# Optimization experiments

Measured on AMD Instinct MI355X. Metric: run time of the kernel, lower is better.

Reference implementation:

```python
import jax, jax.numpy as jnp
import numpy as np

# Dimensions
T, B = 128, 512
NTOK, NINP, NHID = 512, 512, 600
NB, BS, TOPK = 6, 100, 4          # num_blocks, block_size = nhid//num_blocks, update_topk
H, DK, DV, ATT = 4, 64, 85, 340   # input-attention heads, key dim, value dim (H*DV == attention_out)
H2, DK2, DV2 = 4, 32, 32          # communication (step) attention dims


def setup_inputs() -> dict:
    key = jax.random.key(0)
    ks = jax.random.split(key, 16)
    def rn(k, shape, s=0.05):
        return (jax.random.normal(k, shape) * s).astype(jnp.float32)
    return dict(
        input=jax.random.normal(ks[0], (T, B, NTOK), dtype=jnp.float32),
        h0=jnp.zeros((B, NHID), jnp.float32),
        masks=jnp.ones((T, B, 1), jnp.float32),
        enc_W=rn(ks[1], (NTOK, NINP)), enc_b=jnp.zeros((NINP,), jnp.float32),
        Wq_in=rn(ks[2], (BS, H * DK)), Wk_in=rn(ks[3], (NINP, H * DK)), Wv_in=rn(ks[4], (NINP, H * DV)),
        W_ih=rn(ks[5], (NB, ATT, 3 * BS)), W_hh=rn(ks[6], (NB, BS, 3 * BS)),
        b_ih=jnp.zeros((NB, 3 * BS), jnp.float32), b_hh=jnp.zeros((NB, 3 * BS), jnp.float32),
        Wq_c=rn(ks[7], (BS, H2 * DK2)), Wk_c=rn(ks[8], (BS, H2 * DK2)),
        Wv_c=rn(ks[9], (BS, H2 * DV2)), Wo_c=rn(ks[10], (H2 * DV2, BS)),
        dec_W=rn(ks[11], (NHID, NTOK)), dec_b=jnp.zeros((NTOK,), jnp.float32),
    )


def _rim_scan(emb, masks, h0, Wq_in, Wk_in, Wv_in, W_ih, W_hh, b_ih, b_hh,
              Wq_c, Wk_c, Wv_c, Wo_c):
    inv_sdk = 1.0 / np.sqrt(DK).astype(np.float32)
    inv_sdk2 = 1.0 / np.sqrt(DK2).astype(np.float32)

    def step(h, xm):
        xt, mt = xm                      # [B,NINP], [B,1]
        h = h * mt                       # episode-reset gating
        hb = h.reshape(B, NB, BS)
        # --- input attention over {real input, null} slots ---
        slots = jnp.stack([xt, jnp.zeros_like(xt)], axis=1)          # [B,2,NINP]
        k = (slots @ Wk_in).reshape(B, 2, H, DK)
        v = (slots @ Wv_in).reshape(B, 2, H, DV)
        q = (hb @ Wq_in).reshape(B, NB, H, DK)
        att = jax.nn.softmax(jnp.einsum('bnhd,bshd->bnhs', q, k) * inv_sdk, axis=-1)
        act = 1.0 - att[..., 1].mean(-1)                             # [B,NB] attention to real input
        kth = jax.lax.top_k(act, TOPK)[0][:, -1:]
        mask = (act >= kth).astype(h.dtype)                          # [B,NB] top-k block activation
        inp_use = jnp.einsum('bnhs,bshd->bnhd', att, v).reshape(B, NB, ATT)
        # --- block-diagonal GRU update ---
        gi = jnp.einsum('bnd,nde->bne', inp_use, W_ih) + b_ih
        gh = jnp.einsum('bnd,nde->bne', hb, W_hh) + b_hh
        gi_r, gi_z, gi_n = jnp.split(gi, 3, axis=-1)
        gh_r, gh_z, gh_n = jnp.split(gh, 3, axis=-1)
        r = jax.nn.sigmoid(gi_r + gh_r)
        z = jax.nn.sigmoid(gi_z + gh_z)
        n = jnp.tanh(gi_n + r * gh_n)
        hn = (1.0 - z) * n + z * hb
        # --- step (communication) attention across blocks, residual ---
        qc = (hn @ Wq_c).reshape(B, NB, H2, DK2)
        kc = (hn @ Wk_c).reshape(B, NB, H2, DK2)
        vc = (hn @ Wv_c).reshape(B, NB, H2, DV2)
        ac = jax.nn.softmax(jnp.einsum('bnhd,bmhd->bhnm', qc, kc) * inv_sdk2, axis=-1)
        co = jnp.einsum('bhnm,bmhd->bnhd', ac, vc).reshape(B, NB, H2 * DV2) @ Wo_c
        hc = hn + co
        # --- only top-k active blocks are updated ---
        m = mask[..., None]
        hf = (m * hc + (1.0 - m) * hb).reshape(B, NHID)
        return hf, (hf, mask)

    h_last, (hs, bmask) = jax.lax.scan(step, h0, (emb, masks))
    return hs, h_last, bmask


def reference(input, h0, masks, enc_W, enc_b, Wq_in, Wk_in, Wv_in,
              W_ih, W_hh, b_ih, b_hh, Wq_c, Wk_c, Wv_c, Wo_c, dec_W, dec_b):
    emb = input @ enc_W + enc_b                                      # encoder Linear [T,B,NINP]
    hs, h_last, bmask = _rim_scan(emb, masks, h0, Wq_in, Wk_in, Wv_in,
                                  W_ih, W_hh, b_ih, b_hh, Wq_c, Wk_c, Wv_c, Wo_c)
    dec = hs @ dec_W + dec_b                                         # decoder [T,B,NTOK]
    return dec
```

## Files before the change

kernel.cpp:

```cpp
#include <hip/hip_runtime.h>
#include <math.h>

#define T_STEPS 128
#define BATCH   512
#define NTOK    512
#define NINP    512
#define NHID    600
#define NBK     6
#define BS      100
#define HH      4
#define DK      64
#define DV      85
#define ATT     340
#define H2      4
#define DK2     32
#define DV2     32
#define G3      300
#define VN      340
#define KAPN    400
#define CN      740
#define CNP     768
#define UN2     1800
#define UN2P    1920
#define UK0     128
#define KV0     512
#define DECKP   640
#define SW      2

typedef __attribute__((ext_vector_type(8))) short short8;
typedef __attribute__((ext_vector_type(4))) float f32x4;

__device__ __forceinline__ float sigf(float x) { return 1.f / (1.f + expf(-x)); }
__device__ __forceinline__ unsigned short f2b(float f) {
    unsigned u = __float_as_uint(f);
    unsigned r = (u + 0x7fffu + ((u >> 16) & 1u)) >> 16;
    return (unsigned short)r;
}
__device__ __forceinline__ float b2f(unsigned short u) {
    return __uint_as_float(((unsigned)u) << 16);
}
__device__ __forceinline__ void split3(float x, unsigned short& hi,
                                       unsigned short& mid, unsigned short& lo) {
    hi = f2b(x);
    float r1 = x - b2f(hi);
    mid = f2b(r1);
    lo = f2b(r1 - b2f(mid));
}

struct ZOff { int div; long s1; long s2; };
__device__ __forceinline__ long zoff(ZOff z, int bz) {
    return (long)(bz / z.div) * z.s1 + (long)(bz % z.div) * z.s2;
}

__device__ __forceinline__ void swz_decode(int& x, int& y, int& z) {
    int gx = gridDim.x, gy = gridDim.y;
    int flat = (blockIdx.z * gy + blockIdx.y) * gx + blockIdx.x;
    int nwg = gx * gy * gridDim.z;
    int per = nwg >> 3;
    int nf = (flat & 7) * per + (flat >> 3);
    y = nf % gy; int t2 = nf / gy; x = t2 % gx; z = t2 / gx;
}

__global__ __launch_bounds__(256) void gemm6(
    const unsigned short* __restrict__ A, long aZ, int aZdiv,
    const unsigned short* __restrict__ B, long bZ,
    float* __restrict__ C, long cZ, int ldc, int Nreal,
    const float* __restrict__ bias, int K0)
{
    int bx, by, bz;
    swz_decode(bx, by, bz);
    A += (long)(bz / aZdiv) * aZ;
    B += (long)bz * bZ;
    C += (long)bz * cZ;
    const int LDA = 3 * K0;
    const int m0 = by * 128, n0 = bx * 128;
    __shared__ __align__(16) unsigned short As[128 * 64];
    __shared__ __align__(16) unsigned short Bs[128 * 64];
    const int tid = threadIdx.x;
    const int lane = tid & 63;
    const int wid = tid >> 6;
    const int wr = wid >> 1, wc = wid & 1;

    f32x4 acc[4][4];
#pragma unroll
    for (int m = 0; m < 4; m++)
#pragma unroll
        for (int n = 0; n < 4; n++)
#pragma unroll
            for (int v = 0; v < 4; v++) acc[m][n][v] = 0.f;

    const int segA[6] = {0, 0, 1, 0, 2, 1};
    const int segB[6] = {0, 1, 0, 2, 0, 1};
    for (int p = 0; p < 6; p++) {
        const unsigned short* Ap = A + segA[p] * K0;
        const unsigned short* Bp = B + segB[p] * K0;
        for (int k0 = 0; k0 < K0; k0 += 64) {
            short8 ra[4], rb[4];
#pragma unroll
            for (int q = 0; q < 4; q++) {
                int idx = (q << 8) + tid;
                int r = idx >> 3, ce = (idx & 7) << 3;
                ra[q] = *(const short8*)&Ap[(long)(m0 + r) * LDA + k0 + ce];
                rb[q] = *(const short8*)&Bp[(long)(n0 + r) * LDA + k0 + ce];
            }
            __syncthreads();
#pragma unroll
            for (int q = 0; q < 4; q++) {
                int idx = (q << 8) + tid;
                int r = idx >> 3, ce = (idx & 7) << 3;
                *(short8*)&As[r * 64 + ce] = ra[q];
                *(short8*)&Bs[r * 64 + ce] = rb[q];
            }
            __syncthreads();
#pragma unroll
            for (int kk = 0; kk < 2; kk++) {
                short8 af[4], bfr[4];
#pragma unroll
                for (int m = 0; m < 4; m++)
                    af[m] = *(const short8*)&As[(wr * 64 + m * 16 + (lane & 15)) * 64 + kk * 32 + (lane >> 4) * 8];
#pragma unroll
                for (int n = 0; n < 4; n++)
                    bfr[n] = *(const short8*)&Bs[(wc * 64 + n * 16 + (lane & 15)) * 64 + kk * 32 + (lane >> 4) * 8];
#pragma unroll
                for (int m = 0; m < 4; m++)
#pragma unroll
                    for (int n = 0; n < 4; n++)
                        acc[m][n] = __builtin_amdgcn_mfma_f32_16x16x32_bf16(af[m], bfr[n], acc[m][n], 0, 0, 0);
            }
        }
    }
#pragma unroll
    for (int m = 0; m < 4; m++) {
        int rbase = m0 + wr * 64 + m * 16 + (lane >> 4) * 4;
#pragma unroll
        for (int n = 0; n < 4; n++) {
            int col = n0 + wc * 64 + n * 16 + (lane & 15);
            if (col < Nreal) {
                float bv = bias ? bias[col] : 0.f;
#pragma unroll
                for (int v = 0; v < 4; v++)
                    C[(long)(rbase + v) * ldc + col] = acc[m][n][v] + bv;
            }
        }
    }
}

__global__ __launch_bounds__(256) void gemm6_kv(
    const unsigned short* __restrict__ A,
    const unsigned short* __restrict__ B,
    unsigned short* __restrict__ A_U,
    float* __restrict__ Kbuf,
    const float* __restrict__ bias, int K0, int MU)
{
    int bx, by, bz;
    swz_decode(bx, by, bz);
    const int LDA = 3 * K0;
    const int m0 = by * 128, n0 = bx * 128;
    __shared__ __align__(16) unsigned short As[128 * 64];
    __shared__ __align__(16) unsigned short Bs[128 * 64];
    const int tid = threadIdx.x;
    const int lane = tid & 63;
    const int wid = tid >> 6;
    const int wr = wid >> 1, wc = wid & 1;

    f32x4 acc[4][4];
#pragma unroll
    for (int m = 0; m < 4; m++)
#pragma unroll
        for (int n = 0; n < 4; n++)
#pragma unroll
            for (int v = 0; v < 4; v++) acc[m][n][v] = 0.f;

    const int segA[6] = {0, 0, 1, 0, 2, 1};
    const int segB[6] = {0, 1, 0, 2, 0, 1};
    for (int p = 0; p < 6; p++) {
        const unsigned short* Ap = A + segA[p] * K0;
        const unsigned short* Bp = B + segB[p] * K0;
        for (int k0 = 0; k0 < K0; k0 += 64) {
            short8 ra[4], rb[4];
#pragma unroll
            for (int q = 0; q < 4; q++) {
                int idx = (q << 8) + tid;
                int r = idx >> 3, ce = (idx & 7) << 3;
                ra[q] = *(const short8*)&Ap[(long)(m0 + r) * LDA + k0 + ce];
                rb[q] = *(const short8*)&Bp[(long)(n0 + r) * LDA + k0 + ce];
            }
            __syncthreads();
#pragma unroll
            for (int q = 0; q < 4; q++) {
                int idx = (q << 8) + tid;
                int r = idx >> 3, ce = (idx & 7) << 3;
                *(short8*)&As[r * 64 + ce] = ra[q];
                *(short8*)&Bs[r * 64 + ce] = rb[q];
            }
            __syncthreads();
#pragma unroll
            for (int kk = 0; kk < 2; kk++) {
                short8 af[4], bfr[4];
#pragma unroll
                for (int m = 0; m < 4; m++)
                    af[m] = *(const short8*)&As[(wr * 64 + m * 16 + (lane & 15)) * 64 + kk * 32 + (lane >> 4) * 8];
#pragma unroll
                for (int n = 0; n < 4; n++)
                    bfr[n] = *(const short8*)&Bs[(wc * 64 + n * 16 + (lane & 15)) * 64 + kk * 32 + (lane >> 4) * 8];
#pragma unroll
                for (int m = 0; m < 4; m++)
#pragma unroll
                    for (int n = 0; n < 4; n++)
                        acc[m][n] = __builtin_amdgcn_mfma_f32_16x16x32_bf16(af[m], bfr[n], acc[m][n], 0, 0, 0);
            }
        }
    }
#pragma unroll
    for (int m = 0; m < 4; m++) {
        int rbase = m0 + wr * 64 + m * 16 + (lane >> 4) * 4;
#pragma unroll
        for (int n = 0; n < 4; n++) {
            int col = n0 + wc * 64 + n * 16 + (lane & 15);
            if (col < CN) {
                float bv = bias[col];
                if (col < VN) {
                    int h = col / DV, kk2 = col - h * DV;
#pragma unroll
                    for (int v = 0; v < 4; v++) {
                        float val = acc[m][n][v] + bv;
                        unsigned short hi, mid, lo;
                        split3(val, hi, mid, lo);
                        long base = ((long)h * MU + (rbase + v)) * (3 * UK0) + kk2;
                        A_U[base] = hi;
                        A_U[base + UK0] = mid;
                        A_U[base + 2 * UK0] = lo;
                    }
                } else {
                    int kc = col - VN;
#pragma unroll
                    for (int v = 0; v < 4; v++)
                        Kbuf[(long)(rbase + v) * KAPN + kc] = acc[m][n][v] + bv;
                }
            }
        }
    }
}

__global__ __launch_bounds__(256) void gemm_mfma(
    const unsigned short* __restrict__ A,
    const unsigned short* __restrict__ B,
    float* __restrict__ C, int ldc,
    const float* __restrict__ bias, int Kp)
{
    const int m0 = blockIdx.y * 128, n0 = blockIdx.x * 128;
    __shared__ __align__(16) unsigned short As[128 * 64];
    __shared__ __align__(16) unsigned short Bs[128 * 64];
    const int tid = threadIdx.x;
    const int lane = tid & 63;
    const int wid = tid >> 6;
    const int wr = wid >> 1, wc = wid & 1;

    f32x4 acc[4][4];
#pragma unroll
    for (int m = 0; m < 4; m++)
#pragma unroll
        for (int n = 0; n < 4; n++)
#pragma unroll
            for (int v = 0; v < 4; v++) acc[m][n][v] = 0.f;

    for (int k0 = 0; k0 < Kp; k0 += 64) {
        short8 ra[4], rb[4];
#pragma unroll
        for (int q = 0; q < 4; q++) {
            int idx = (q << 8) + tid;
            int r = idx >> 3, ce = (idx & 7) << 3;
            ra[q] = *(const short8*)&A[(long)(m0 + r) * Kp + k0 + ce];
            rb[q] = *(const short8*)&B[(long)(n0 + r) * Kp + k0 + ce];
        }
        __syncthreads();
#pragma unroll
        for (int q = 0; q < 4; q++) {
            int idx = (q << 8) + tid;
            int r = idx >> 3, ce = (idx & 7) << 3;
            *(short8*)&As[r * 64 + ce] = ra[q];
            *(short8*)&Bs[r * 64 + ce] = rb[q];
        }
        __syncthreads();
#pragma unroll
        for (int kk = 0; kk < 2; kk++) {
            short8 af[4], bfr[4];
#pragma unroll
            for (int m = 0; m < 4; m++)
                af[m] = *(const short8*)&As[(wr * 64 + m * 16 + (lane & 15)) * 64 + kk * 32 + (lane >> 4) * 8];
#pragma unroll
            for (int n = 0; n < 4; n++)
                bfr[n] = *(const short8*)&Bs[(wc * 64 + n * 16 + (lane & 15)) * 64 + kk * 32 + (lane >> 4) * 8];
#pragma unroll
            for (int m = 0; m < 4; m++)
#pragma unroll
                for (int n = 0; n < 4; n++)
                    acc[m][n] = __builtin_amdgcn_mfma_f32_16x16x32_bf16(af[m], bfr[n], acc[m][n], 0, 0, 0);
        }
    }
#pragma unroll
    for (int m = 0; m < 4; m++) {
        int rbase = m0 + wr * 64 + m * 16 + (lane >> 4) * 4;
#pragma unroll
        for (int n = 0; n < 4; n++) {
            int col = n0 + wc * 64 + n * 16 + (lane & 15);
            float bv = bias ? bias[col] : 0.f;
#pragma unroll
            for (int v = 0; v < 4; v++)
                C[(long)(rbase + v) * ldc + col] = acc[m][n][v] + bv;
        }
    }
}

__global__ __launch_bounds__(256) void sgemm(
    const float* __restrict__ A, ZOff za, int lda,
    const float* __restrict__ B, ZOff zb, int ldb,
    float* __restrict__ C, ZOff zc, int ldc,
    int M, int N, int K)
{
    const int bz = blockIdx.z;
    A += zoff(za, bz);
    B += zoff(zb, bz);
    C += zoff(zc, bz);
    const int m0 = blockIdx.y * 128, n0 = blockIdx.x * 64;
    __shared__ float As[16][132];
    __shared__ float Bs[16][68];
    const int tid = threadIdx.x;
    const int tm = tid >> 4, tn = tid & 15;
    const int ar = tid >> 1, ak = (tid & 1) * 8;
    const int bk = tid >> 4, bn = (tid & 15) * 4;

    float acc[8][4];
#pragma unroll
    for (int i = 0; i < 8; i++)
#pragma unroll
        for (int j = 0; j < 4; j++) acc[i][j] = 0.f;

    for (int k0 = 0; k0 < K; k0 += 16) {
        float av[8], bv[4];
#pragma unroll
        for (int j = 0; j < 8; j++) {
            int gk = k0 + ak + j;
            av[j] = (gk < K) ? A[(long)(m0 + ar) * lda + gk] : 0.f;
        }
#pragma unroll
        for (int j = 0; j < 4; j++) {
            int gk = k0 + bk, gn = n0 + bn + j;
            bv[j] = (gk < K && gn < N) ? B[(long)gk * ldb + gn] : 0.f;
        }
        __syncthreads();
#pragma unroll
        for (int j = 0; j < 8; j++) As[ak + j][ar] = av[j];
#pragma unroll
        for (int j = 0; j < 4; j++) Bs[bk][bn + j] = bv[j];
        __syncthreads();
#pragma unroll
        for (int kk = 0; kk < 16; kk++) {
            float a[8], b[4];
#pragma unroll
            for (int i = 0; i < 8; i++) a[i] = As[kk][tm * 8 + i];
#pragma unroll
            for (int j = 0; j < 4; j++) b[j] = Bs[kk][tn * 4 + j];
#pragma unroll
            for (int i = 0; i < 8; i++)
#pragma unroll
                for (int j = 0; j < 4; j++)
                    acc[i][j] += a[i] * b[j];
        }
    }
#pragma unroll
    for (int i = 0; i < 8; i++) {
        int gm = m0 + tm * 8 + i;
#pragma unroll
        for (int j = 0; j < 4; j++) {
            int gn = n0 + tn * 4 + j;
            if (gn < N) C[(long)gm * ldc + gn] = acc[i][j];
        }
    }
}

__global__ __launch_bounds__(256) void prep_wqt(const float* __restrict__ Wq_in,
                                                float* __restrict__ WqT)
{
    int idx = blockIdx.x * 256 + threadIdx.x;
    if (idx >= HH * DK * BS) return;
    int h = idx / (DK * BS), r = idx - h * DK * BS, d = r / BS, w = r - d * BS;
    WqT[idx] = Wq_in[w * (HH * DK) + h * DK + d];
}

__global__ __launch_bounds__(256) void prep_whh4(const float* __restrict__ W_hh,
                                                 float* __restrict__ Whh4)
{
    int idx = blockIdx.x * 256 + threadIdx.x;
    if (idx >= NBK * BS * G3) return;
    int n = idx / (BS * G3), r = idx - n * (BS * G3);
    int d = r / G3, e = r - d * G3;
    int g = e / BS, w = e - g * BS;
    Whh4[(((long)n * BS + d) * BS + w) * 4 + g] = W_hh[idx];
}

__global__ __launch_bounds__(256) void bias_k(const float* __restrict__ enc_b,
                                              const float* __restrict__ Wk,
                                              float* __restrict__ kbf)
{
    int j = threadIdx.x;
    if (j >= HH * DK) return;
    float acc = 0.f;
    for (int d = 0; d < NINP; d++) acc += enc_b[d] * Wk[d * (HH * DK) + j];
    kbf[j] = acc;
}

__global__ __launch_bounds__(256) void bias_c_kernel(const float* __restrict__ enc_b,
                                                     const float* __restrict__ Wv,
                                                     const float* __restrict__ kbf,
                                                     const float* __restrict__ WqT,
                                                     float* __restrict__ bias_c)
{
    int j = blockIdx.x * 256 + threadIdx.x;
    if (j >= CNP) return;
    float acc = 0.f;
    if (j < VN) {
        for (int d = 0; d < NINP; d++) acc += enc_b[d] * Wv[d * (HH * DV) + j];
    } else if (j < CN) {
        int r = j - VN;
        int h = r / BS, w = r - h * BS;
        for (int d = 0; d < DK; d++)
            acc += kbf[h * DK + d] * WqT[(h * DK + d) * BS + w];
    }
    bias_c[j] = acc;
}

__global__ __launch_bounds__(256) void cvt_dec(const float* __restrict__ dec_W,
                                               unsigned short* __restrict__ dst)
{
    int idx = blockIdx.x * 256 + threadIdx.x;
    if (idx >= NTOK * DECKP) return;
    int n = idx / DECKP, k = idx - n * DECKP;
    dst[idx] = f2b(k < NHID ? dec_W[k * NTOK + n] : 0.f);
}

__global__ __launch_bounds__(256) void cvt_split_ew(const float* __restrict__ EWfull,
                                                    unsigned short* __restrict__ dst)
{
    int idx = blockIdx.x * 256 + threadIdx.x;
    if (idx >= CNP * NTOK) return;
    int n = idx / NTOK, k = idx - n * NTOK;
    float x = (n < CN) ? EWfull[(long)k * CNP + n] : 0.f;
    unsigned short hi, mid, lo;
    split3(x, hi, mid, lo);
    long base = (long)n * (3 * KV0) + k;
    dst[base] = hi;
    dst[base + KV0] = mid;
    dst[base + 2 * KV0] = lo;
}

__global__ __launch_bounds__(256) void cvt_split_bu2(const float* __restrict__ W_ih,
                                                     unsigned short* __restrict__ dst)
{
    int idx = blockIdx.x * 256 + threadIdx.x;
    if (idx >= HH * UN2P * UK0) return;
    int h = idx / (UN2P * UK0), r = idx - h * (UN2P * UK0);
    int j = r / UK0, kk = r - j * UK0;
    float x = 0.f;
    if (kk < DV && j < UN2) {
        int n = j / G3, e = j - n * G3;
        x = W_ih[((long)n * ATT + h * DV + kk) * G3 + e];
    }
    unsigned short hi, mid, lo;
    split3(x, hi, mid, lo);
    long base = ((long)h * UN2P + j) * (3 * UK0) + kk;
    dst[base] = hi;
    dst[base + UK0] = mid;
    dst[base + 2 * UK0] = lo;
}

__global__ __launch_bounds__(256) void cvt_split_in(const float* __restrict__ src,
                                                    unsigned short* __restrict__ dst, long rows)
{
    long total = rows * NTOK;
    long i = (long)blockIdx.x * 256 + threadIdx.x;
    long stride = (long)gridDim.x * 256;
    for (; i < total; i += stride) {
        long row = i / NTOK; int k = (int)(i - row * NTOK);
        unsigned short hi, mid, lo;
        split3(src[i], hi, mid, lo);
        long base = row * (3 * KV0) + k;
        dst[base] = hi;
        dst[base + KV0] = mid;
        dst[base + 2 * KV0] = lo;
    }
}

__global__ __launch_bounds__(1024) void step_fused(
    const float* __restrict__ h_prev,
    const float* __restrict__ masks_t,
    const float* __restrict__ Kbuf,
    const float* __restrict__ U,
    const float* __restrict__ b_ih, const float* __restrict__ b_hh,
    const float* __restrict__ Whh4,
    const float* __restrict__ Wq_c, const float* __restrict__ Wk_c,
    const float* __restrict__ Wv_c, const float* __restrict__ Wo_c,
    float* __restrict__ h_out,
    unsigned short* __restrict__ A_dec,
    int s_step, int MU)
{
    const int b0 = blockIdx.x * SW, tid = threadIdx.x;
    __shared__ __align__(16) float hbT[NHID][SW];
    __shared__ __align__(16) float hnT[NHID][SW];
    __shared__ __align__(16) float kp[SW][KAPN];
    __shared__ __align__(16) float qcb[SW][768], kcb[SW][768], vcb[SW][768];
    __shared__ __align__(16) float coT[NBK * 128][SW];
    __shared__ float part[SW * 96];
    __shared__ float att[SW][24], mk[SW][NBK];
    __shared__ float lg[SW][144];

    const long rowd0 = (long)s_step * BATCH + b0;

    for (int i = tid; i < SW * NHID; i += 1024) {
        int s = i / NHID, j = i - s * NHID;
        hbT[j][s] = h_prev[(long)(b0 + s) * NHID + j] * masks_t[b0 + s];
    }
    for (int i = tid; i < SW * KAPN; i += 1024) {
        int s = i / KAPN, j = i - s * KAPN;
        kp[s][j] = Kbuf[(rowd0 + s) * KAPN + j];
    }
    __syncthreads();
    if (tid < SW * 96) {
        int g = tid >> 2, q = tid & 3;
        int s = g / 24, r = g - s * 24;
        int n = r >> 2, h = r & 3;
        float acc = 0.f;
        int w0 = q * 25;
        for (int w = w0; w < w0 + 25; w++) acc += hbT[n * BS + w][s] * kp[s][h * BS + w];
        part[tid] = acc;
    }
    __syncthreads();
    if (tid < SW * 24) {
        int s = tid / 24, r = tid - s * 24;
        float l = part[tid * 4] + part[tid * 4 + 1] + part[tid * 4 + 2] + part[tid * 4 + 3];
        att[s][r] = sigf(l * 0.125f);
    }
    __syncthreads();
    if (tid < SW) {
        float a[NBK], av[NBK];
        for (int n = 0; n < NBK; n++) {
            av[n] = 0.25f * (att[tid][n * 4] + att[tid][n * 4 + 1] + att[tid][n * 4 + 2] + att[tid][n * 4 + 3]);
            a[n] = av[n];
        }
        for (int i = 0; i < 4; i++) {
            int mx = i;
            for (int j = i + 1; j < NBK; j++) if (a[j] > a[mx]) mx = j;
            float t = a[i]; a[i] = a[mx]; a[mx] = t;
        }
        float kth = a[3];
        for (int n = 0; n < NBK; n++) mk[tid][n] = (av[n] >= kth) ? 1.f : 0.f;
    }

    if (tid < 600) {
        const int n2 = tid / 100, w2 = tid - n2 * 100;
        float gi[3][SW], gh[3][SW];
#pragma unroll
        for (int g = 0; g < 3; g++) {
            float bi = b_ih[n2 * G3 + g * BS + w2];
            float bh = b_hh[n2 * G3 + g * BS + w2];
#pragma unroll
            for (int s = 0; s < SW; s++) { gi[g][s] = bi; gh[g][s] = bh; }
        }
#pragma unroll
        for (int h = 0; h < HH; h++) {
            const float* Uh = U + ((long)h * MU + rowd0) * UN2 + n2 * G3;
#pragma unroll
            for (int s = 0; s < SW; s++) {
                float a = att[s][n2 * 4 + h];
#pragma unroll
                for (int g = 0; g < 3; g++)
                    gi[g][s] += a * Uh[(long)s * UN2 + g * BS + w2];
            }
        }
        const f32x4* Wn4 = ((const f32x4*)Whh4) + (long)n2 * BS * BS + w2;
#pragma unroll 4
        for (int d = 0; d < BS; d++) {
            f32x4 wv = Wn4[(long)d * BS];
            float2 hv = *(const float2*)&hbT[n2 * BS + d][0];
            gh[0][0] += wv[0] * hv.x; gh[0][1] += wv[0] * hv.y;
            gh[1][0] += wv[1] * hv.x; gh[1][1] += wv[1] * hv.y;
            gh[2][0] += wv[2] * hv.x; gh[2][1] += wv[2] * hv.y;
        }
        float2 hnv;
        {
            float rr0 = sigf(gi[0][0] + gh[0][0]);
            float zz0 = sigf(gi[1][0] + gh[1][0]);
            float ng0 = tanhf(gi[2][0] + rr0 * gh[2][0]);
            hnv.x = (1.f - zz0) * ng0 + zz0 * hbT[n2 * BS + w2][0];
            float rr1 = sigf(gi[0][1] + gh[0][1]);
            float zz1 = sigf(gi[1][1] + gh[1][1]);
            float ng1 = tanhf(gi[2][1] + rr1 * gh[2][1]);
            hnv.y = (1.f - zz1) * ng1 + zz1 * hbT[n2 * BS + w2][1];
        }
        *(float2*)&hnT[n2 * BS + w2][0] = hnv;
    }
    __syncthreads();

    if (tid < 768) {
        const int mat = tid >> 8, r = tid & 255, ng = r >> 7, c = r & 127;
        const float* W = (mat == 0) ? Wq_c : ((mat == 1) ? Wk_c : Wv_c);
        float acc[3][SW];
#pragma unroll
        for (int j = 0; j < 3; j++)
#pragma unroll
            for (int s = 0; s < SW; s++) acc[j][s] = 0.f;
#pragma unroll 4
        for (int d = 0; d < BS; d++) {
            float wv = W[d * 128 + c];
#pragma unroll
            for (int j = 0; j < 3; j++) {
                float2 hv = *(const float2*)&hnT[(ng * 3 + j) * BS + d][0];
                acc[j][0] += wv * hv.x;
                acc[j][1] += wv * hv.y;
            }
        }
        float (*dst)[768] = (mat == 0) ? qcb : ((mat == 1) ? kcb : vcb);
#pragma unroll
        for (int j = 0; j < 3; j++)
#pragma unroll
            for (int s = 0; s < SW; s++)
                dst[s][(ng * 3 + j) * 128 + c] = acc[j][s];
    }
    __syncthreads();

    if (tid < SW * 144) {
        int s = tid / 144, r = tid - s * 144;
        int h = r / 36, r2 = r - h * 36, n = r2 / NBK, m = r2 - n * NBK;
        float sv = 0.f;
#pragma unroll
        for (int e4 = 0; e4 < 8; e4++) {
            f32x4 qv = *(const f32x4*)&qcb[s][n * 128 + h * 32 + e4 * 4];
            f32x4 kv = *(const f32x4*)&kcb[s][m * 128 + h * 32 + e4 * 4];
            sv += qv[0] * kv[0] + qv[1] * kv[1] + qv[2] * kv[2] + qv[3] * kv[3];
        }
        lg[s][r] = sv * 0.17677669529663687f;
    }
    __syncthreads();
    if (tid < SW * 24) {
        int s = tid / 24, r = tid - s * 24;
        float* row = &lg[s][r * NBK];
        float mx = row[0];
        for (int m = 1; m < NBK; m++) mx = fmaxf(mx, row[m]);
        float sv = 0.f;
        for (int m = 0; m < NBK; m++) { row[m] = expf(row[m] - mx); sv += row[m]; }
        float inv = 1.f / sv;
        for (int m = 0; m < NBK; m++) row[m] *= inv;
    }
    __syncthreads();
    for (int idx = tid; idx < SW * 768; idx += 1024) {
        int s = idx / 768, r = idx - s * 768;
        int n = r >> 7, d = r & 127, h = d >> 5;
        float a = 0.f;
#pragma unroll
        for (int m = 0; m < NBK; m++) a += lg[s][h * 36 + n * NBK + m] * vcb[s][m * 128 + d];
        coT[r][s] = a;
    }
    __syncthreads();

    if (tid < 600) {
        const int n2 = tid / 100, w2 = tid - n2 * 100;
        float a0 = 0.f, a1 = 0.f;
#pragma unroll 4
        for (int d = 0; d < 128; d++) {
            float wv = Wo_c[d * BS + w2];
            float2 cv = *(const float2*)&coT[n2 * 128 + d][0];
            a0 += wv * cv.x;
            a1 += wv * cv.y;
        }
        float2 res;
        float hc0 = hnT[n2 * BS + w2][0] + a0;
        float hc1 = hnT[n2 * BS + w2][1] + a1;
        res.x = (mk[0][n2] > 0.5f) ? hc0 : hbT[n2 * BS + w2][0];
        res.y = (mk[1][n2] > 0.5f) ? hc1 : hbT[n2 * BS + w2][1];
        *(float2*)&hbT[n2 * BS + w2][0] = res;
    }
    __syncthreads();
    for (int i = tid; i < SW * NHID; i += 1024) {
        int s = i / NHID, j = i - s * NHID;
        h_out[(long)(b0 + s) * NHID + j] = hbT[j][s];
    }
    for (int i = tid; i < SW * DECKP; i += 1024) {
        int s = i / DECKP, col = i - s * DECKP;
        A_dec[(rowd0 + s) * DECKP + col] = f2b(col < NHID ? hbT[col][s] : 0.f);
    }
}

extern "C" void kernel_launch(void* const* d_in, const int* in_sizes, int n_in,
                              void* d_out, int out_size, void* d_ws, size_t ws_size,
                              hipStream_t stream)
{
    const float* input = (const float*)d_in[0];
    const float* h0    = (const float*)d_in[1];
    const float* masks = (const float*)d_in[2];
    const float* enc_W = (const float*)d_in[3];
    const float* enc_b = (const float*)d_in[4];
    const float* Wq_in = (const float*)d_in[5];
    const float* Wk_in = (const float*)d_in[6];
    const float* Wv_in = (const float*)d_in[7];
    const float* W_ih  = (const float*)d_in[8];
    const float* W_hh  = (const float*)d_in[9];
    const float* b_ih  = (const float*)d_in[10];
    const float* b_hh  = (const float*)d_in[11];
    const float* Wq_c  = (const float*)d_in[12];
    const float* Wk_c  = (const float*)d_in[13];
    const float* Wv_c  = (const float*)d_in[14];
    const float* Wo_c  = (const float*)d_in[15];
    const float* dec_W = (const float*)d_in[16];
    const float* dec_b = (const float*)d_in[17];
    float* out = (float*)d_out;

    const size_t AL = 256;
    auto pad = [&](size_t x) { return (x + AL - 1) & ~(AL - 1); };
    size_t fixedB = pad((size_t)NTOK * CNP * 4)
                  + pad((size_t)NTOK * 256 * 4)
                  + pad((size_t)HH * DK * BS * 4)
                  + pad((size_t)256 * 4)
                  + pad((size_t)CNP * 4)
                  + pad((size_t)NBK * BS * BS * 4 * 4)
                  + pad((size_t)CNP * 3 * KV0 * 2)
                  + pad((size_t)HH * UN2P * 3 * UK0 * 2)
                  + pad((size_t)NTOK * DECKP * 2)
                  + 2 * pad((size_t)BATCH * NHID * 4);
    auto perC = [&](int C) {
        size_t MU = (size_t)C * BATCH;
        return pad(MU * 3 * KV0 * 2)
             + pad(MU * KAPN * 4)
             + pad((size_t)HH * MU * 3 * UK0 * 2)
             + pad((size_t)HH * MU * UN2 * 4)
             + pad(MU * DECKP * 2);
    };
    int C = 8;
    while (C > 1 && fixedB + perC(C) > ws_size) C >>= 1;
    const int MU = C * BATCH;
    const int NCH = T_STEPS / C;

    char* p = (char*)d_ws;
    auto alloc = [&](size_t bytes) { char* r = p; p += pad(bytes); return r; };
    float*          EWfull = (float*)alloc((size_t)NTOK * CNP * 4);
    float*          EWk    = (float*)alloc((size_t)NTOK * 256 * 4);
    float*          WqT    = (float*)alloc((size_t)HH * DK * BS * 4);
    float*          kbf    = (float*)alloc((size_t)256 * 4);
    float*          bias_c = (float*)alloc((size_t)CNP * 4);
    float*          Whh4   = (float*)alloc((size_t)NBK * BS * BS * 4 * 4);
    unsigned short* B_vkap = (unsigned short*)alloc((size_t)CNP * 3 * KV0 * 2);
    unsigned short* B_U    = (unsigned short*)alloc((size_t)HH * UN2P * 3 * UK0 * 2);
    unsigned short* B_dec  = (unsigned short*)alloc((size_t)NTOK * DECKP * 2);
    float*          hA     = (float*)alloc((size_t)BATCH * NHID * 4);
    float*          hB     = (float*)alloc((size_t)BATCH * NHID * 4);
    unsigned short* A_in   = (unsigned short*)alloc((size_t)MU * 3 * KV0 * 2);
    float*          Kbuf   = (float*)alloc((size_t)MU * KAPN * 4);
    unsigned short* A_U    = (unsigned short*)alloc((size_t)HH * MU * 3 * UK0 * 2);
    float*          Ubuf   = (float*)alloc((size_t)HH * MU * UN2 * 4);
    unsigned short* A_dec  = (unsigned short*)alloc((size_t)MU * DECKP * 2);

    dim3 blk(256);
    ZOff z0 = {1, 0, 0};

    sgemm<<<dim3(6, 4, 1), blk, 0, stream>>>(
        enc_W, z0, NINP, Wv_in, z0, HH * DV, EWfull, z0, CNP, NTOK, VN, NINP);
    sgemm<<<dim3(4, 4, 1), blk, 0, stream>>>(
        enc_W, z0, NINP, Wk_in, z0, HH * DK, EWk, z0, 256, NTOK, HH * DK, NINP);
    prep_wqt<<<dim3((HH * DK * BS + 255) / 256), blk, 0, stream>>>(Wq_in, WqT);
    prep_whh4<<<dim3((NBK * BS * G3 + 255) / 256), blk, 0, stream>>>(W_hh, Whh4);
    sgemm<<<dim3(2, 4, HH), blk, 0, stream>>>(
        EWk, ZOff{1, DK, 0}, 256, WqT, ZOff{1, (long)DK * BS, 0}, BS,
        EWfull + VN, ZOff{1, BS, 0}, CNP, NTOK, BS, DK);
    bias_k<<<dim3(1), blk, 0, stream>>>(enc_b, Wk_in, kbf);
    bias_c_kernel<<<dim3(3), blk, 0, stream>>>(enc_b, Wv_in, kbf, WqT, bias_c);
    cvt_split_ew<<<dim3((CNP * NTOK + 255) / 256), blk, 0, stream>>>(EWfull, B_vkap);
    cvt_split_bu2<<<dim3((HH * UN2P * UK0 + 255) / 256), blk, 0, stream>>>(W_ih, B_U);
    cvt_dec<<<dim3((NTOK * DECKP + 255) / 256), blk, 0, stream>>>(dec_W, B_dec);

    const float* hp = h0;
    float* hbufs[2] = { hA, hB };
    int t = 0;
    for (int c = 0; c < NCH; c++) {
        cvt_split_in<<<dim3(2048), blk, 0, stream>>>(
            input + (size_t)c * MU * NTOK, A_in, MU);
        gemm6_kv<<<dim3(CNP / 128, MU / 128, 1), blk, 0, stream>>>(
            A_in, B_vkap, A_U, Kbuf, bias_c, KV0, MU);
        gemm6<<<dim3(UN2P / 128, MU / 128, HH), blk, 0, stream>>>(
            A_U, (long)MU * 3 * UK0, 1, B_U, (long)UN2P * 3 * UK0,
            Ubuf, (long)MU * UN2, UN2, UN2, nullptr, UK0);
        for (int s = 0; s < C; s++, t++) {
            float* hout = hbufs[t & 1];
            step_fused<<<dim3(BATCH / SW), dim3(1024), 0, stream>>>(
                hp, masks + (size_t)t * BATCH, Kbuf, Ubuf, b_ih, b_hh, Whh4,
                Wq_c, Wk_c, Wv_c, Wo_c, hout, A_dec, s, MU);
            hp = hout;
        }
        gemm_mfma<<<dim3(NTOK / 128, MU / 128, 1), blk, 0, stream>>>(
            A_dec, B_dec, out + (size_t)c * MU * NTOK, NTOK, dec_b, DECKP);
    }
}
```

Before: 6.537 ms.

## Prefetch U rows early in step kernel, drop GEMM block swizzle, raise unroll factors

The per-step recurrent kernel now loads its 24 U values per thread into registers at kernel start, before the shared-memory staging and attention phases, so the global-load latency overlaps earlier work. The XCD-aware block index swizzle is removed from both GEMM kernels in favour of plain blockIdx mapping. Unroll factors of the inner matvec loops are increased. The extra live registers and the loss of the L2-friendly block ordering could reduce occupancy or cache locality.

```diff
diff --git a/kernel.cpp b/kernel.cpp
--- a/kernel.cpp
+++ b/kernel.cpp
@@ -52,28 +52,18 @@
     return (long)(bz / z.div) * z.s1 + (long)(bz % z.div) * z.s2;
 }
 
-__device__ __forceinline__ void swz_decode(int& x, int& y, int& z) {
-    int gx = gridDim.x, gy = gridDim.y;
-    int flat = (blockIdx.z * gy + blockIdx.y) * gx + blockIdx.x;
-    int nwg = gx * gy * gridDim.z;
-    int per = nwg >> 3;
-    int nf = (flat & 7) * per + (flat >> 3);
-    y = nf % gy; int t2 = nf / gy; x = t2 % gx; z = t2 / gx;
-}
-
 __global__ __launch_bounds__(256) void gemm6(
     const unsigned short* __restrict__ A, long aZ, int aZdiv,
     const unsigned short* __restrict__ B, long bZ,
     float* __restrict__ C, long cZ, int ldc, int Nreal,
     const float* __restrict__ bias, int K0)
 {
-    int bx, by, bz;
-    swz_decode(bx, by, bz);
+    const int bz = blockIdx.z;
     A += (long)(bz / aZdiv) * aZ;
     B += (long)bz * bZ;
     C += (long)bz * cZ;
     const int LDA = 3 * K0;
-    const int m0 = by * 128, n0 = bx * 128;
+    const int m0 = blockIdx.y * 128, n0 = blockIdx.x * 128;
     __shared__ __align__(16) unsigned short As[128 * 64];
     __shared__ __align__(16) unsigned short Bs[128 * 64];
     const int tid = threadIdx.x;
@@ -152,10 +142,8 @@
     float* __restrict__ Kbuf,
     const float* __restrict__ bias, int K0, int MU)
 {
-    int bx, by, bz;
-    swz_decode(bx, by, bz);
     const int LDA = 3 * K0;
-    const int m0 = by * 128, n0 = bx * 128;
+    const int m0 = blockIdx.y * 128, n0 = blockIdx.x * 128;
     __shared__ __align__(16) unsigned short As[128 * 64];
     __shared__ __align__(16) unsigned short Bs[128 * 64];
     const int tid = threadIdx.x;
@@ -515,6 +503,21 @@
     __shared__ float lg[SW][144];
 
     const long rowd0 = (long)s_step * BATCH + b0;
+    const int n2 = (tid < 600) ? tid / 100 : 0;
+    const int w2 = (tid < 600) ? tid - n2 * 100 : 0;
+
+    float uraw[HH][3][SW];
+    if (tid < 600) {
+#pragma unroll
+        for (int h = 0; h < HH; h++) {
+            const float* Uh = U + ((long)h * MU + rowd0) * UN2 + n2 * G3;
+#pragma unroll
+            for (int s = 0; s < SW; s++)
+#pragma unroll
+                for (int g = 0; g < 3; g++)
+                    uraw[h][g][s] = Uh[(long)s * UN2 + g * BS + w2];
+        }
+    }
 
     for (int i = tid; i < SW * NHID; i += 1024) {
         int s = i / NHID, j = i - s * NHID;
@@ -557,7 +560,6 @@
     }
 
     if (tid < 600) {
-        const int n2 = tid / 100, w2 = tid - n2 * 100;
         float gi[3][SW], gh[3][SW];
 #pragma unroll
         for (int g = 0; g < 3; g++) {
@@ -567,18 +569,16 @@
             for (int s = 0; s < SW; s++) { gi[g][s] = bi; gh[g][s] = bh; }
         }
 #pragma unroll
-        for (int h = 0; h < HH; h++) {
-            const float* Uh = U + ((long)h * MU + rowd0) * UN2 + n2 * G3;
+        for (int h = 0; h < HH; h++)
 #pragma unroll
             for (int s = 0; s < SW; s++) {
                 float a = att[s][n2 * 4 + h];
 #pragma unroll
                 for (int g = 0; g < 3; g++)
-                    gi[g][s] += a * Uh[(long)s * UN2 + g * BS + w2];
-            }
-        }
+                    gi[g][s] += a * uraw[h][g][s];
+            }
         const f32x4* Wn4 = ((const f32x4*)Whh4) + (long)n2 * BS * BS + w2;
-#pragma unroll 4
+#pragma unroll 10
         for (int d = 0; d < BS; d++) {
             f32x4 wv = Wn4[(long)d * BS];
             float2 hv = *(const float2*)&hbT[n2 * BS + d][0];
@@ -609,7 +609,7 @@
         for (int j = 0; j < 3; j++)
 #pragma unroll
             for (int s = 0; s < SW; s++) acc[j][s] = 0.f;
-#pragma unroll 4
+#pragma unroll 10
         for (int d = 0; d < BS; d++) {
             float wv = W[d * 128 + c];
 #pragma unroll
@@ -663,9 +663,8 @@
     __syncthreads();
 
     if (tid < 600) {
-        const int n2 = tid / 100, w2 = tid - n2 * 100;
         float a0 = 0.f, a1 = 0.f;
-#pragma unroll 4
+#pragma unroll 8
         for (int d = 0; d < 128; d++) {
             float wv = Wo_c[d * BS + w2];
             float2 cv = *(const float2*)&coT[n2 * 128 + d][0];
```

New measurement: 6.374 ms. 1.03x faster.
